# Kernel optimization log

Hardware: AMD Instinct MI355X
Metric: run time of the kernel (lower is better)

Reference implementation:

```python
import jax, jax.numpy as jnp
import numpy as np

N_NODES = 50000
N_EDGES = 800000
IN_DIM = 256
OUT_DIM = 32
NUM_HEADS = 8


def setup_inputs() -> dict:
    key = jax.random.key(0)
    ks = jax.random.split(key, 9)
    h = jax.random.normal(ks[0], (N_NODES, IN_DIM), dtype=jnp.float32)
    src = jax.random.randint(ks[1], (N_EDGES,), 0, N_NODES, dtype=jnp.int32)
    dst = jax.random.randint(ks[2], (N_EDGES,), 0, N_NODES, dtype=jnp.int32)
    s = 1.0 / np.sqrt(IN_DIM)
    W_lin = jax.random.uniform(ks[3], (IN_DIM, IN_DIM), jnp.float32, -s, s)
    b_lin = jax.random.uniform(ks[4], (IN_DIM,), jnp.float32, -s, s)
    # DGL GATConv fc: Linear(in_feats, out_feats*num_heads, bias=False)
    W_gat = jax.random.normal(ks[5], (IN_DIM, NUM_HEADS * OUT_DIM), dtype=jnp.float32) * s
    attn_l = jax.random.normal(ks[6], (NUM_HEADS, OUT_DIM), dtype=jnp.float32) * 0.1
    attn_r = jax.random.normal(ks[7], (NUM_HEADS, OUT_DIM), dtype=jnp.float32) * 0.1
    gat_bias = jnp.zeros((NUM_HEADS * OUT_DIM,), dtype=jnp.float32)
    return {"h": h, "src": src, "dst": dst, "W_lin": W_lin, "b_lin": b_lin,
            "W_gat": W_gat, "attn_l": attn_l, "attn_r": attn_r, "gat_bias": gat_bias}


def reference(h, src, dst, W_lin, b_lin, W_gat, attn_l, attn_r, gat_bias):
    N = h.shape[0]
    # pre-linear (nn.Linear(in_dim, in_dim))
    h = h @ W_lin + b_lin                                   # [N, in_dim]
    h_in = h
    # GATConv (eval mode: feat_drop/attn_drop are identity)
    feat = (h @ W_gat).reshape(N, NUM_HEADS, OUT_DIM)       # [N, H, D]
    el = jnp.sum(feat * attn_l, axis=-1)                    # [N, H]
    er = jnp.sum(feat * attn_r, axis=-1)                    # [N, H]
    e = jax.nn.leaky_relu(el[src] + er[dst], 0.2)           # [E, H]  (DGL slope 0.2)
    # edge softmax normalized over incoming edges of each dst node
    m = jax.ops.segment_max(e, dst, num_segments=N)         # [N, H]
    m = jnp.where(jnp.isfinite(m), m, 0.0)                  # guard empty segments
    e = jnp.exp(e - m[dst])                                 # [E, H]
    s = jax.ops.segment_sum(e, dst, num_segments=N)         # [N, H]
    a = e / s[dst]                                          # [E, H]
    # weighted neighbor aggregation
    msg = feat[src] * a[:, :, None]                         # [E, H, D]
    out = jax.ops.segment_sum(msg, dst, num_segments=N)     # [N, H, D]
    out = out.reshape(N, NUM_HEADS * OUT_DIM) + gat_bias
    # GATLayer activation: F.leaky_relu (default slope 0.01), then residual
    out = jax.nn.leaky_relu(out, 0.01)
    return h_in + out
```

## Files before the change

kernel.cpp:

```cpp
#include <hip/hip_runtime.h>
#include <math.h>

#define NN 50000
#define NE 800000
#define DIM 256
#define NH 8
#define HD 32
#define CAP 64
#define GEMM_GRID ((NN + 63) / 64)
#define SCAT_GRID ((NE / 4 + 255) / 256)

typedef __attribute__((ext_vector_type(8))) short bf16x8;
typedef __attribute__((ext_vector_type(4))) float f32x4;
typedef unsigned short u16;

__device__ __forceinline__ u16 f2bf(float f) {
    unsigned u = __float_as_uint(f);
    return (u16)((u + 0x7FFFu + ((u >> 16) & 1u)) >> 16);
}

__device__ __forceinline__ void pack_body(int b, const float* __restrict__ Wl,
    const float* __restrict__ Wg, u16* __restrict__ Bl, u16* __restrict__ Bg)
{
    const float* W = (b < 256) ? Wl : Wg;
    u16* Bp = (b < 256) ? Bl : Bg;
    int idx = (b & 255) * 256 + threadIdx.x;
    int j    = idx & 7;
    int lane = (idx >> 3) & 63;
    int ks   = (idx >> 9) & 7;
    int nf   = idx >> 12;
    int n = nf * 16 + (lane & 15);
    int k = ks * 32 + (lane >> 4) * 8 + j;
    Bp[idx] = f2bf(W[k * 256 + n]);
}

__global__ __launch_bounds__(256) void k_scatter_pack(
    const int* __restrict__ src, const int* __restrict__ dst,
    int* __restrict__ deg, int* __restrict__ csr_pad,
    const float* __restrict__ Wl, const float* __restrict__ Wg,
    u16* __restrict__ Bl, u16* __restrict__ Bg)
{
    int bid = blockIdx.x;
    if (bid < SCAT_GRID) {
        int e0 = (bid * 256 + threadIdx.x) * 4;
        if (e0 >= NE) return;
        int4 sv = *(const int4*)(src + e0);
        int4 dv = *(const int4*)(dst + e0);
        int p;
        p = atomicAdd(&deg[dv.x], 1); if (p < CAP) csr_pad[dv.x * CAP + p] = sv.x;
        p = atomicAdd(&deg[dv.y], 1); if (p < CAP) csr_pad[dv.y * CAP + p] = sv.y;
        p = atomicAdd(&deg[dv.z], 1); if (p < CAP) csr_pad[dv.z * CAP + p] = sv.z;
        p = atomicAdd(&deg[dv.w], 1); if (p < CAP) csr_pad[dv.w * CAP + p] = sv.w;
    } else {
        pack_body(bid - SCAT_GRID, Wl, Wg, Bl, Bg);
    }
}

template<int AF32, int DO_ELER, int HAS_BIAS>
__device__ void gemm_body(int bid, const void* __restrict__ A,
    const u16* __restrict__ Bp, const float* __restrict__ bias,
    u16* __restrict__ Cb, const float* __restrict__ attn_l,
    const float* __restrict__ attn_r, float* __restrict__ el,
    float* __restrict__ er, int M, u16* Bs)
{
    const int t    = threadIdx.x;
    const int lane = t & 63;
    const int wid  = t >> 6;
    const int row0 = bid * 64 + wid * 16;
    const int arow = min(row0 + (lane & 15), M - 1);
    const int kgrp = lane >> 4;

    bf16x8 af[8];
    if (AF32) {
        const float* ap = (const float*)A + (size_t)arow * DIM + kgrp * 8;
        #pragma unroll
        for (int ks = 0; ks < 8; ++ks) {
            float4 x = *(const float4*)(ap + ks * 32);
            float4 y = *(const float4*)(ap + ks * 32 + 4);
            bf16x8 v;
            v[0] = (short)f2bf(x.x); v[1] = (short)f2bf(x.y);
            v[2] = (short)f2bf(x.z); v[3] = (short)f2bf(x.w);
            v[4] = (short)f2bf(y.x); v[5] = (short)f2bf(y.y);
            v[6] = (short)f2bf(y.z); v[7] = (short)f2bf(y.w);
            af[ks] = v;
        }
    } else {
        const u16* ap = (const u16*)A + (size_t)arow * DIM + kgrp * 8;
        #pragma unroll
        for (int ks = 0; ks < 8; ++ks)
            af[ks] = *(const bf16x8*)(ap + ks * 32);
    }

    const int crow0 = row0 + (lane >> 4) * 4;
    const int ccol  = lane & 15;

    uint4 v0, v1, v2, v3;
    {
        const uint4* p = (const uint4*)Bp + t;
        v0 = p[0]; v1 = p[256]; v2 = p[512]; v3 = p[768];
    }

    for (int c = 0; c < 8; ++c) {
        {
            uint4* q = (uint4*)Bs + t;
            q[0] = v0; q[256] = v1; q[512] = v2; q[768] = v3;
        }
        if (c < 7) {
            const uint4* p = (const uint4*)(Bp + (size_t)(c + 1) * 8192) + t;
            v0 = p[0]; v1 = p[256]; v2 = p[512]; v3 = p[768];
        }
        __syncthreads();

        f32x4 acc0 = (f32x4){0.f, 0.f, 0.f, 0.f};
        f32x4 acc1 = (f32x4){0.f, 0.f, 0.f, 0.f};
        const u16* ls = Bs + lane * 8;
        #pragma unroll
        for (int ks = 0; ks < 8; ++ks) {
            bf16x8 b0 = *(const bf16x8*)(ls + (size_t)ks * 512);
            bf16x8 b1 = *(const bf16x8*)(ls + (size_t)(8 + ks) * 512);
            acc0 = __builtin_amdgcn_mfma_f32_16x16x32_bf16(af[ks], b0, acc0, 0, 0, 0);
            acc1 = __builtin_amdgcn_mfma_f32_16x16x32_bf16(af[ks], b1, acc1, 0, 0, 0);
        }

        {
            int col0 = c * 32 + ccol;
            int col1 = col0 + 16;
            float bv0 = HAS_BIAS ? bias[col0] : 0.f;
            float bv1 = HAS_BIAS ? bias[col1] : 0.f;
            #pragma unroll
            for (int r = 0; r < 4; ++r) {
                int row = crow0 + r;
                if (row < M) {
                    Cb[(size_t)row * DIM + col0] = f2bf(acc0[r] + bv0);
                    Cb[(size_t)row * DIM + col1] = f2bf(acc1[r] + bv1);
                }
            }
        }

        if (DO_ELER) {
            float al0 = attn_l[c * HD + ccol], al1 = attn_l[c * HD + ccol + 16];
            float ar0 = attn_r[c * HD + ccol], ar1 = attn_r[c * HD + ccol + 16];
            float ep[4], rp[4];
            #pragma unroll
            for (int r = 0; r < 4; ++r) {
                ep[r] = acc0[r] * al0 + acc1[r] * al1;
                rp[r] = acc0[r] * ar0 + acc1[r] * ar1;
            }
            #pragma unroll
            for (int off = 1; off < 16; off <<= 1) {
                #pragma unroll
                for (int r = 0; r < 4; ++r) {
                    ep[r] += __shfl_xor(ep[r], off, 64);
                    rp[r] += __shfl_xor(rp[r], off, 64);
                }
            }
            int rsel = ccol & 3;
            float ev = (rsel == 0) ? ep[0] : (rsel == 1) ? ep[1] : (rsel == 2) ? ep[2] : ep[3];
            float rv = (rsel == 0) ? rp[0] : (rsel == 1) ? rp[1] : (rsel == 2) ? rp[2] : rp[3];
            int row = crow0 + rsel;
            if (ccol < 4)      { if (row < M) el[(size_t)row * NH + c] = ev; }
            else if (ccol < 8) { if (row < M) er[(size_t)row * NH + c] = rv; }
        }
        __syncthreads();
    }
}

__global__ __launch_bounds__(256) void k_gemm1(
    const float* __restrict__ h, const u16* __restrict__ Bp1,
    const float* __restrict__ b_lin, u16* __restrict__ h1b)
{
    __shared__ u16 Bs[8192];
    gemm_body<1, 0, 1>(blockIdx.x, h, Bp1, b_lin, h1b,
                       nullptr, nullptr, nullptr, nullptr, NN, Bs);
}

__global__ __launch_bounds__(256) void k_gemm2(
    const u16* __restrict__ h1b, const u16* __restrict__ Bp2,
    u16* __restrict__ featb, const float* __restrict__ attn_l,
    const float* __restrict__ attn_r, float* __restrict__ el,
    float* __restrict__ er)
{
    __shared__ u16 Bs[8192];
    gemm_body<0, 1, 0>(blockIdx.x, h1b, Bp2, nullptr, featb,
                       attn_l, attn_r, el, er, NN, Bs);
}

#define BODYR(j)                                                         \
    {                                                                    \
        int   s  = __shfl(s_l, base32 + j0 + (j), 64);                   \
        float wv = __shfl((j) < 4 ? w0 : w1,                             \
                          base32 + ((j) & 3) * 8 + myhead, 64);          \
        uint4 fv = *(const uint4*)(featb + (size_t)s * DIM + c);         \
        acc0 += __uint_as_float(fv.x << 16)         * wv;                \
        acc1 += __uint_as_float(fv.x & 0xFFFF0000u) * wv;                \
        acc2 += __uint_as_float(fv.y << 16)         * wv;                \
        acc3 += __uint_as_float(fv.y & 0xFFFF0000u) * wv;                \
        acc4 += __uint_as_float(fv.z << 16)         * wv;                \
        acc5 += __uint_as_float(fv.z & 0xFFFF0000u) * wv;                \
        acc6 += __uint_as_float(fv.w << 16)         * wv;                \
        acc7 += __uint_as_float(fv.w & 0xFFFF0000u) * wv;                \
        sw   += wv;                                                      \
    }

__global__ __launch_bounds__(256) void aggregate_hw(
    const int* __restrict__ deg, const int* __restrict__ csr_pad,
    const float* __restrict__ el, const float* __restrict__ er,
    const u16* __restrict__ featb, const u16* __restrict__ h1b,
    const float* __restrict__ bias, float* __restrict__ out)
{
    const int t      = threadIdx.x;
    const int hl     = t & 31;
    const int d      = blockIdx.x * 8 + (t >> 5);
    const int myhead = hl >> 2;
    const int c      = hl * 8;
    const int base32 = t & 32;
    const int cnt  = min(deg[d], CAP);
    const int* ebase = csr_pad + (size_t)d * CAP;
    const float er_p = er[(size_t)d * NH + (hl & 7)];

    float acc0 = 0.f, acc1 = 0.f, acc2 = 0.f, acc3 = 0.f;
    float acc4 = 0.f, acc5 = 0.f, acc6 = 0.f, acc7 = 0.f, sw = 0.f;

    for (int base = 0; base < cnt; base += 32) {
        const int nb = min(32, cnt - base);
        int s_l = (hl < nb) ? ebase[base + hl] : 0;
        for (int j0 = 0; j0 < nb; j0 += 8) {
            const int m = min(8, nb - j0);
            int e0 = min(j0 + (hl >> 3), nb - 1);
            int e1 = min(j0 + 4 + (hl >> 3), nb - 1);
            int se0 = __shfl(s_l, base32 + e0, 64);
            int se1 = __shfl(s_l, base32 + e1, 64);
            float x0 = el[(size_t)se0 * NH + (hl & 7)] + er_p;
            float x1 = el[(size_t)se1 * NH + (hl & 7)] + er_p;
            x0 = x0 > 0.f ? x0 : 0.2f * x0;
            x1 = x1 > 0.f ? x1 : 0.2f * x1;
            float w0 = __expf(x0);
            float w1 = __expf(x1);
            if (m == 8) {
                int ss[8];
                #pragma unroll
                for (int j = 0; j < 8; ++j) ss[j] = __shfl(s_l, base32 + j0 + j, 64);
                uint4 fv[8];
                #pragma unroll
                for (int j = 0; j < 8; ++j)
                    fv[j] = *(const uint4*)(featb + (size_t)ss[j] * DIM + c);
                #pragma unroll
                for (int j = 0; j < 8; ++j) {
                    float wv = __shfl(j < 4 ? w0 : w1,
                                      base32 + (j & 3) * 8 + myhead, 64);
                    acc0 += __uint_as_float(fv[j].x << 16)         * wv;
                    acc1 += __uint_as_float(fv[j].x & 0xFFFF0000u) * wv;
                    acc2 += __uint_as_float(fv[j].y << 16)         * wv;
                    acc3 += __uint_as_float(fv[j].y & 0xFFFF0000u) * wv;
                    acc4 += __uint_as_float(fv[j].z << 16)         * wv;
                    acc5 += __uint_as_float(fv[j].z & 0xFFFF0000u) * wv;
                    acc6 += __uint_as_float(fv[j].w << 16)         * wv;
                    acc7 += __uint_as_float(fv[j].w & 0xFFFF0000u) * wv;
                    sw   += wv;
                }
            } else {
                for (int j = 0; j < m; ++j) BODYR(j)
            }
        }
    }

    const float rs = (cnt > 0) ? 1.f / sw : 0.f;
    uint4  hv = *(const uint4*)(h1b + (size_t)d * DIM + c);
    float4 b0 = *(const float4*)(bias + c);
    float4 b1 = *(const float4*)(bias + c + 4);
    float r;
    float4 o0, o1;
    r = acc0 * rs + b0.x; r = r > 0.f ? r : 0.01f * r; o0.x = __uint_as_float(hv.x << 16)         + r;
    r = acc1 * rs + b0.y; r = r > 0.f ? r : 0.01f * r; o0.y = __uint_as_float(hv.x & 0xFFFF0000u) + r;
    r = acc2 * rs + b0.z; r = r > 0.f ? r : 0.01f * r; o0.z = __uint_as_float(hv.y << 16)         + r;
    r = acc3 * rs + b0.w; r = r > 0.f ? r : 0.01f * r; o0.w = __uint_as_float(hv.y & 0xFFFF0000u) + r;
    r = acc4 * rs + b1.x; r = r > 0.f ? r : 0.01f * r; o1.x = __uint_as_float(hv.z << 16)         + r;
    r = acc5 * rs + b1.y; r = r > 0.f ? r : 0.01f * r; o1.y = __uint_as_float(hv.z & 0xFFFF0000u) + r;
    r = acc6 * rs + b1.z; r = r > 0.f ? r : 0.01f * r; o1.z = __uint_as_float(hv.w << 16)         + r;
    r = acc7 * rs + b1.w; r = r > 0.f ? r : 0.01f * r; o1.w = __uint_as_float(hv.w & 0xFFFF0000u) + r;
    *(float4*)(out + (size_t)d * DIM + c)     = o0;
    *(float4*)(out + (size_t)d * DIM + c + 4) = o1;
}

extern "C" void kernel_launch(void* const* d_in, const int* in_sizes, int n_in,
                              void* d_out, int out_size, void* d_ws, size_t ws_size,
                              hipStream_t stream)
{
    const float* h      = (const float*)d_in[0];
    const int*   src    = (const int*)d_in[1];
    const int*   dst    = (const int*)d_in[2];
    const float* W_lin  = (const float*)d_in[3];
    const float* b_lin  = (const float*)d_in[4];
    const float* W_gat  = (const float*)d_in[5];
    const float* attn_l = (const float*)d_in[6];
    const float* attn_r = (const float*)d_in[7];
    const float* g_bias = (const float*)d_in[8];
    float* out = (float*)d_out;

    u16*   h1b    = (u16*)d_ws;
    u16*   featb  = h1b + (size_t)NN * DIM;
    u16*   Bp_lin = featb + (size_t)NN * DIM;
    u16*   Bp_gat = Bp_lin + 65536;
    float* el     = (float*)(Bp_gat + 65536);
    float* er     = el + (size_t)NN * NH;
    int*   deg     = (int*)(er + (size_t)NN * NH);
    int*   csr_pad = deg + NN + 8;

    hipMemsetAsync(deg, 0, (size_t)NN * sizeof(int), stream);

    k_scatter_pack<<<SCAT_GRID + 512, 256, 0, stream>>>(src, dst, deg, csr_pad,
                                                        W_lin, W_gat, Bp_lin, Bp_gat);
    k_gemm1<<<GEMM_GRID, 256, 0, stream>>>(h, Bp_lin, b_lin, h1b);
    k_gemm2<<<GEMM_GRID, 256, 0, stream>>>(h1b, Bp_gat, featb, attn_l, attn_r, el, er);
    aggregate_hw<<<NN / 8, 256, 0, stream>>>(deg, csr_pad, el, er, featb,
                                             h1b, g_bias, out);
}
```

Before: 181.0 us.

## Overlap edge scatter with first GEMM and fold deg zeroing into pack kernel

The separate memset of the degree array is removed and the zeroing moves into the weight-pack kernel as extra blocks. The edge scatter (atomic CSR build) moves out of the pack kernel and into the first GEMM launch as extra blocks, so the atomic-heavy scatter can run alongside the GEMM. This drops one launch and lets the memory-bound scatter overlap the compute-bound GEMM. The cost is that the two block types compete for CU resources, and the scatter blocks carry the GEMM's shared memory allocation.

```diff
diff --git a/kernel.cpp b/kernel.cpp
--- a/kernel.cpp
+++ b/kernel.cpp
@@ -19,40 +19,26 @@
     return (u16)((u + 0x7FFFu + ((u >> 16) & 1u)) >> 16);
 }
 
-__device__ __forceinline__ void pack_body(int b, const float* __restrict__ Wl,
-    const float* __restrict__ Wg, u16* __restrict__ Bl, u16* __restrict__ Bg)
-{
-    const float* W = (b < 256) ? Wl : Wg;
-    u16* Bp = (b < 256) ? Bl : Bg;
-    int idx = (b & 255) * 256 + threadIdx.x;
-    int j    = idx & 7;
-    int lane = (idx >> 3) & 63;
-    int ks   = (idx >> 9) & 7;
-    int nf   = idx >> 12;
-    int n = nf * 16 + (lane & 15);
-    int k = ks * 32 + (lane >> 4) * 8 + j;
-    Bp[idx] = f2bf(W[k * 256 + n]);
-}
-
-__global__ __launch_bounds__(256) void k_scatter_pack(
-    const int* __restrict__ src, const int* __restrict__ dst,
-    int* __restrict__ deg, int* __restrict__ csr_pad,
+__global__ __launch_bounds__(256) void k_pack_zero(
     const float* __restrict__ Wl, const float* __restrict__ Wg,
-    u16* __restrict__ Bl, u16* __restrict__ Bg)
-{
-    int bid = blockIdx.x;
-    if (bid < SCAT_GRID) {
-        int e0 = (bid * 256 + threadIdx.x) * 4;
-        if (e0 >= NE) return;
-        int4 sv = *(const int4*)(src + e0);
-        int4 dv = *(const int4*)(dst + e0);
-        int p;
-        p = atomicAdd(&deg[dv.x], 1); if (p < CAP) csr_pad[dv.x * CAP + p] = sv.x;
-        p = atomicAdd(&deg[dv.y], 1); if (p < CAP) csr_pad[dv.y * CAP + p] = sv.y;
-        p = atomicAdd(&deg[dv.z], 1); if (p < CAP) csr_pad[dv.z * CAP + p] = sv.z;
-        p = atomicAdd(&deg[dv.w], 1); if (p < CAP) csr_pad[dv.w * CAP + p] = sv.w;
+    u16* __restrict__ Bl, u16* __restrict__ Bg, int* __restrict__ deg)
+{
+    int b = blockIdx.x;
+    if (b < 512) {
+        const float* W = (b < 256) ? Wl : Wg;
+        u16* Bp = (b < 256) ? Bl : Bg;
+        int idx = (b & 255) * 256 + threadIdx.x;
+        int j    = idx & 7;
+        int lane = (idx >> 3) & 63;
+        int ks   = (idx >> 9) & 7;
+        int nf   = idx >> 12;
+        int n = nf * 16 + (lane & 15);
+        int k = ks * 32 + (lane >> 4) * 8 + j;
+        Bp[idx] = f2bf(W[k * 256 + n]);
     } else {
-        pack_body(bid - SCAT_GRID, Wl, Wg, Bl, Bg);
+        int i = (b - 512) * 256 + threadIdx.x;
+        if (i < NN / 4)
+            ((int4*)deg)[i] = (int4){0, 0, 0, 0};
     }
 }
 
@@ -165,13 +151,28 @@
     }
 }
 
-__global__ __launch_bounds__(256) void k_gemm1(
+__global__ __launch_bounds__(256) void k_gemm1_scatter(
     const float* __restrict__ h, const u16* __restrict__ Bp1,
-    const float* __restrict__ b_lin, u16* __restrict__ h1b)
+    const float* __restrict__ b_lin, u16* __restrict__ h1b,
+    const int* __restrict__ src, const int* __restrict__ dst,
+    int* __restrict__ deg, int* __restrict__ csr_pad)
 {
     __shared__ u16 Bs[8192];
-    gemm_body<1, 0, 1>(blockIdx.x, h, Bp1, b_lin, h1b,
-                       nullptr, nullptr, nullptr, nullptr, NN, Bs);
+    int bid = blockIdx.x;
+    if (bid < GEMM_GRID) {
+        gemm_body<1, 0, 1>(bid, h, Bp1, b_lin, h1b,
+                           nullptr, nullptr, nullptr, nullptr, NN, Bs);
+    } else {
+        int e0 = ((bid - GEMM_GRID) * 256 + threadIdx.x) * 4;
+        if (e0 >= NE) return;
+        int4 sv = *(const int4*)(src + e0);
+        int4 dv = *(const int4*)(dst + e0);
+        int p;
+        p = atomicAdd(&deg[dv.x], 1); if (p < CAP) csr_pad[dv.x * CAP + p] = sv.x;
+        p = atomicAdd(&deg[dv.y], 1); if (p < CAP) csr_pad[dv.y * CAP + p] = sv.y;
+        p = atomicAdd(&deg[dv.z], 1); if (p < CAP) csr_pad[dv.z * CAP + p] = sv.z;
+        p = atomicAdd(&deg[dv.w], 1); if (p < CAP) csr_pad[dv.w * CAP + p] = sv.w;
+    }
 }
 
 __global__ __launch_bounds__(256) void k_gemm2(
@@ -306,11 +307,9 @@
     int*   deg     = (int*)(er + (size_t)NN * NH);
     int*   csr_pad = deg + NN + 8;
 
-    hipMemsetAsync(deg, 0, (size_t)NN * sizeof(int), stream);
-
-    k_scatter_pack<<<SCAT_GRID + 512, 256, 0, stream>>>(src, dst, deg, csr_pad,
-                                                        W_lin, W_gat, Bp_lin, Bp_gat);
-    k_gemm1<<<GEMM_GRID, 256, 0, stream>>>(h, Bp_lin, b_lin, h1b);
+    k_pack_zero<<<512 + 64, 256, 0, stream>>>(W_lin, W_gat, Bp_lin, Bp_gat, deg);
+    k_gemm1_scatter<<<GEMM_GRID + SCAT_GRID, 256, 0, stream>>>(
+        h, Bp_lin, b_lin, h1b, src, dst, deg, csr_pad);
     k_gemm2<<<GEMM_GRID, 256, 0, stream>>>(h1b, Bp_gat, featb, attn_l, attn_r, el, er);
     aggregate_hw<<<NN / 8, 256, 0, stream>>>(deg, csr_pad, el, er, featb,
                                              h1b, g_bias, out);
```

Measured after the change: 166.4 us. -8.1%, faster.
